# Optimization experiments

Measured on AMD Instinct MI355X. Metric: run time of the kernel, lower is better.

## Reference

```python
import jax, jax.numpy as jnp
import numpy as np

B = 65536
NODE, ENUM, ETYPE = 4, 6, 5
XDIM, EDIM, HDIM, ZDIM = 4, 5, 128, 32
ODIM = (2 * NODE + ETYPE) * ENUM  # 78
BETA = 0.005
EPS_SCALE = 0.01


def setup_inputs() -> dict:
    keys = jax.random.split(jax.random.key(0), 64)
    ki = iter(range(64))
    def rn(shape, s=1.0):
        return jax.random.normal(keys[next(ki)], shape, dtype=jnp.float32) * s
    # NAS-Bench-201 DAG edges per graph, batched as disjoint union
    base_src = jnp.array([0, 0, 1, 0, 1, 2], dtype=jnp.int32)
    base_dst = jnp.array([1, 2, 2, 3, 3, 3], dtype=jnp.int32)
    off = (jnp.arange(B, dtype=jnp.int32) * NODE)[:, None]
    edge_index = jnp.stack([(off + base_src).reshape(-1), (off + base_dst).reshape(-1)])
    s = 0.05
    inp = {
        'x': rn((B * NODE, XDIM)),
        'edge_attr': rn((B * ENUM, EDIM)),
        'arch_tensor': jax.random.uniform(keys[next(ki)], (B, ENUM, 2 * NODE + ETYPE), dtype=jnp.float32),
        'eps': rn((B, ZDIM)),
        'edge_index': edge_index,
        # conv0 (xdim=4 -> hdim=128)
        'c0_rw1': rn((XDIM, XDIM), s), 'c0_rb1': jnp.zeros((XDIM,), jnp.float32),
        'c0_rw2': rn((XDIM, HDIM), s), 'c0_rb2': jnp.zeros((HDIM,), jnp.float32),
        'c0_kw': rn((2 * XDIM + EDIM, HDIM), s),
        # conv1, conv2 (128 -> 128)
        'c1_rw1': rn((HDIM, HDIM), s), 'c1_rb1': jnp.zeros((HDIM,), jnp.float32),
        'c1_rw2': rn((HDIM, HDIM), s), 'c1_rb2': jnp.zeros((HDIM,), jnp.float32),
        'c1_kw': rn((2 * HDIM + EDIM, HDIM), s),
        'c2_rw1': rn((HDIM, HDIM), s), 'c2_rb1': jnp.zeros((HDIM,), jnp.float32),
        'c2_rw2': rn((HDIM, HDIM), s), 'c2_rb2': jnp.zeros((HDIM,), jnp.float32),
        'c2_kw': rn((2 * HDIM + EDIM, HDIM), s),
        # VAE heads
        'fc3_w': rn((HDIM, ZDIM), s), 'fc3_b': jnp.zeros((ZDIM,), jnp.float32),
        'fc4_w': rn((HDIM, ZDIM), s), 'fc4_b': jnp.zeros((ZDIM,), jnp.float32),
        'fc5_w': rn((ZDIM, HDIM), s), 'fc5_b': jnp.zeros((HDIM,), jnp.float32),
        # decoder: Resid_MLP(hdim,hdim) -> Resid_MLP(hdim,odim)
        'd1_mw': rn((HDIM, HDIM), s), 'd1_mb': jnp.zeros((HDIM,), jnp.float32),
        'd1_rw': rn((HDIM, HDIM), s), 'd1_rb': jnp.zeros((HDIM,), jnp.float32),
        'd2_mw': rn((HDIM, ODIM), s), 'd2_mb': jnp.zeros((ODIM,), jnp.float32),
        'd2_rw': rn((HDIM, ODIM), s), 'd2_rb': jnp.zeros((ODIM,), jnp.float32),
    }
    return inp


def _ce(logits, labels):
    # mean cross-entropy over batch*edges, like F.cross_entropy(..., reduction='mean')
    ls = jax.nn.log_softmax(logits, axis=-1)
    return -jnp.mean(jnp.take_along_axis(ls, labels[..., None], axis=-1))


def reference(x, edge_attr, arch_tensor, eps, edge_index,
              c0_rw1, c0_rb1, c0_rw2, c0_rb2, c0_kw,
              c1_rw1, c1_rb1, c1_rw2, c1_rb2, c1_kw,
              c2_rw1, c2_rb1, c2_rw2, c2_rb2, c2_kw,
              fc3_w, fc3_b, fc4_w, fc4_b, fc5_w, fc5_b,
              d1_mw, d1_mb, d1_rw, d1_rb, d2_mw, d2_mb, d2_rw, d2_rb):
    src, dst = edge_index[0], edge_index[1]
    n_nodes = x.shape[0]

    def conv(h, rw1, rb1, rw2, rb2, kw):
        resid = (h @ rw1 + rb1) @ rw2 + rb2  # residual_mlp: two Linears, no activation
        # message: leaky_relu(Linear(cat[x_i(target), x_j(source), edge_attr]))
        m = jax.nn.leaky_relu(jnp.concatenate([h[dst], h[src], edge_attr], axis=1) @ kw)
        return resid + jax.ops.segment_sum(m, dst, num_segments=n_nodes)  # aggr='add'

    h = conv(x, c0_rw1, c0_rb1, c0_rw2, c0_rb2, c0_kw)
    h = conv(h, c1_rw1, c1_rb1, c1_rw2, c1_rb2, c1_kw)
    h = conv(h, c2_rw1, c2_rb1, c2_rw2, c2_rb2, c2_kw)

    hg = h.reshape(B, NODE, HDIM).sum(axis=1)  # sum-pool nodes per graph
    mu = hg @ fc3_w + fc3_b
    logvar = hg @ fc4_w + fc4_b

    # reparameterize (training): z = (eps*eps_scale)*std + mu
    z = eps * EPS_SCALE * jnp.exp(0.5 * logvar) + mu

    # decode
    Hg = jnp.tanh(z @ fc5_w + fc5_b)
    h1 = jax.nn.leaky_relu(Hg @ d1_mw + d1_mb) + (Hg @ d1_rw + d1_rb)
    pred = jax.nn.leaky_relu(h1 @ d2_mw + d2_mb) + (h1 @ d2_rw + d2_rb)
    pred = pred.reshape(B, ENUM, 2 * NODE + ETYPE)
    in_pred, out_pred, et_pred = pred[:, :, :NODE], pred[:, :, NODE:2 * NODE], pred[:, :, 2 * NODE:]

    ti = jnp.argmax(arch_tensor[:, :, :NODE], axis=2)
    to = jnp.argmax(arch_tensor[:, :, NODE:2 * NODE], axis=2)
    te = jnp.argmax(arch_tensor[:, :, 2 * NODE:], axis=2)

    res = _ce(et_pred, te) + _ce(in_pred, ti) + _ce(out_pred, to)
    kld = -0.5 * jnp.mean(1.0 + logvar - mu ** 2 - jnp.exp(logvar))
    return res + BETA * kld
```

## Files before the change

### kernel.cpp

```cpp
#include <hip/hip_runtime.h>
#include <hip/hip_bf16.h>

#define BATCH 65536

typedef __bf16 bf16_t;
typedef __bf16 bf16x8 __attribute__((ext_vector_type(8)));
typedef float  f32x4  __attribute__((ext_vector_type(4)));

__device__ __forceinline__ f32x4 mfma16(bf16x8 a, bf16x8 b, f32x4 c) {
    return __builtin_amdgcn_mfma_f32_16x16x32_bf16(a, b, c, 0, 0, 0);
}
__device__ __forceinline__ int swz128(int row, int col) {
    return row * 128 + ((((col >> 3) ^ (row & 7)) << 3) | (col & 7));
}

struct PrepSrcs { const float* p[16]; };

__global__ __launch_bounds__(256) void prep_weights(PrepSrcs ps,
    const float* __restrict__ c0_rb1, const float* __restrict__ c0_rb2,
    const float* __restrict__ c1_rb1, const float* __restrict__ c1_rb2,
    const float* __restrict__ c2_rb1, const float* __restrict__ c2_rb2,
    bf16_t* __restrict__ dst, float* __restrict__ bias)
{
    int f = blockIdx.x;
    if (f >= 368) {
        int c = threadIdx.x;
        if (c < 128) {
            if (f == 368) {
                const float* rw2 = ps.p[11];
                float s = c1_rb2[c];
                for (int m = 0; m < 128; m++) s += c1_rb1[m] * rw2[m * 128 + c];
                bias[c] = s;
            } else if (f == 369) {
                const float* rw2 = ps.p[13];
                float s = c2_rb2[c];
                for (int m = 0; m < 128; m++) s += c2_rb1[m] * rw2[m * 128 + c];
                bias[128 + c] = s;
            } else {
                const float* rw2 = ps.p[15];
                float s = c0_rb2[c];
                for (int m = 0; m < 4; m++) s += c0_rb1[m] * rw2[m * 128 + c];
                bias[256 + c] = s;
            }
        }
        return;
    }
    const int BASE[20] = {0,32,64,96,128,160,192,200,208,216,248,280,300,320,328,336,344,352,360,368};
    const int SRC[19]  = {10,0,0,12,1,1,2,3,4,5,6,7,8,14,9,9,9,0,1};
    const int KTt[19]  = {4,4,4,4,4,4,4,4,1,4,4,4,4,1,1,1,1,1,1};
    const int KLIM[19] = {128,128,128,128,128,128,128,128,32,128,128,128,128,4,4,4,5,5,5};
    const int NLIM[19] = {128,128,128,128,128,128,32,32,128,128,128,78,78,128,128,128,128,128,128};
    const int STR[19]  = {128,128,128,128,128,128,32,32,128,128,128,78,78,128,128,128,128,128,128};
    const int RO[19]   = {0,0,128,0,0,128,0,0,0,0,0,0,0,0,0,4,8,256,256};

    int ei = 0;
    while (ei < 18 && BASE[ei + 1] <= f) ei++;
    int lf = f - BASE[ei];
    int kt = lf % KTt[ei];
    int nt = lf / KTt[ei];
    #pragma unroll
    for (int r2 = 0; r2 < 2; r2++) {
        int idx = threadIdx.x * 2 + r2;
        int l = idx >> 3, j = idx & 7;
        int row = 32 * kt + 8 * (l >> 4) + j;
        int col = 16 * nt + (l & 15);
        float v = 0.f;
        if (ei == 0 || ei == 3) {
            const float* rw1 = ps.p[ei == 0 ? 10 : 12];
            const float* rw2 = ps.p[ei == 0 ? 11 : 13];
            for (int m = 0; m < 128; m++) v += rw1[row * 128 + m] * rw2[m * 128 + col];
        } else if (ei == 13) {
            if (row < 4) {
                const float* rw1 = ps.p[14];
                const float* rw2 = ps.p[15];
                for (int m = 0; m < 4; m++) v += rw1[row * 4 + m] * rw2[m * 128 + col];
            }
        } else {
            if (row < KLIM[ei] && col < NLIM[ei])
                v = ps.p[SRC[ei]][(row + RO[ei]) * STR[ei] + col];
        }
        dst[f * 512 + idx] = (bf16_t)v;
    }
}

__device__ __forceinline__ void edge_update(float o[4], const f32x4& kd, const f32x4& ks,
                                            const float* et)
{
    float mm;
    mm = kd[1] + ks[0] + et[0]; mm = fmaxf(mm, 0.01f * mm); o[1] += mm;
    mm = kd[2] + ks[0] + et[1]; mm = fmaxf(mm, 0.01f * mm); o[2] += mm;
    mm = kd[2] + ks[1] + et[2]; mm = fmaxf(mm, 0.01f * mm); o[2] += mm;
    mm = kd[3] + ks[0] + et[3]; mm = fmaxf(mm, 0.01f * mm); o[3] += mm;
    mm = kd[3] + ks[1] + et[4]; mm = fmaxf(mm, 0.01f * mm); o[3] += mm;
    mm = kd[3] + ks[2] + et[5]; mm = fmaxf(mm, 0.01f * mm); o[3] += mm;
}

__device__ __forceinline__ void compute_et(bf16_t* etb, const bf16x8* aet,
                                           const bf16_t* wet, int nt,
                                           int w, int q, int lr, int lane)
{
    bf16x8 be = *(const bf16x8*)(wet + nt * 512 + lane * 8);
    #pragma unroll
    for (int t = 0; t < 3; t++) {
        f32x4 z = {0.f, 0.f, 0.f, 0.f};
        z = mfma16(aet[t], be, z);
        #pragma unroll
        for (int j = 0; j < 4; j++)
            etb[(48 * w + 16 * t + 4 * q + j) * 20 + lr] = (bf16_t)z[j];
    }
}

template<bool LAST>
__device__ __forceinline__ void conv_pass(
    bf16_t* lA, bf16_t* etb, const bf16x8* aet,
    const bf16_t* wf, const bf16_t* wet, const float* b12,
    int w, int q, int lr, int lane)
{
    bf16x8 ah[2][4];
    #pragma unroll
    for (int mt = 0; mt < 2; mt++) {
        int row = 32 * w + 16 * mt + lr;
        #pragma unroll
        for (int kt = 0; kt < 4; kt++)
            ah[mt][kt] = *(const bf16x8*)(lA + row * 128 + (((4 * kt + q) ^ (row & 7)) << 3));
    }
    __syncthreads();

    const bf16_t* wfd = wf + 32 * 512;
    const bf16_t* wfs = wf + 64 * 512;
    #pragma unroll 1
    for (int nt = 0; nt < 8; nt++) {
        int col = 16 * nt + lr;
        compute_et(etb, aet, wet, nt, w, q, lr, lane);
        float bv = b12[col];
        f32x4 rr[2], kd[2], ks[2];
        rr[0] = (f32x4){bv, bv, bv, bv}; rr[1] = rr[0];
        kd[0] = (f32x4){0.f, 0.f, 0.f, 0.f}; kd[1] = kd[0];
        ks[0] = kd[0]; ks[1] = kd[0];
        #pragma unroll
        for (int kt = 0; kt < 4; kt++) {
            bf16x8 bw = *(const bf16x8*)(wf  + (nt * 4 + kt) * 512 + lane * 8);
            bf16x8 bd = *(const bf16x8*)(wfd + (nt * 4 + kt) * 512 + lane * 8);
            bf16x8 bs = *(const bf16x8*)(wfs + (nt * 4 + kt) * 512 + lane * 8);
            #pragma unroll
            for (int mt = 0; mt < 2; mt++) {
                rr[mt] = mfma16(ah[mt][kt], bw, rr[mt]);
                kd[mt] = mfma16(ah[mt][kt], bd, kd[mt]);
                ks[mt] = mfma16(ah[mt][kt], bs, ks[mt]);
            }
        }
        #pragma unroll
        for (int mt = 0; mt < 2; mt++) {
            int el = 8 * w + 4 * mt + q;
            float et6[6];
            #pragma unroll
            for (int u = 0; u < 6; u++)
                et6[u] = (float)etb[(48 * w + 24 * mt + 6 * q + u) * 20 + lr];
            float o[4] = {rr[mt][0], rr[mt][1], rr[mt][2], rr[mt][3]};
            edge_update(o, kd[mt], ks[mt], et6);
            if (!LAST) {
                #pragma unroll
                for (int j = 0; j < 4; j++)
                    lA[swz128(32 * w + 16 * mt + 4 * q + j, col)] = (bf16_t)o[j];
            } else {
                lA[swz128(el, col)] = (bf16_t)(o[0] + o[1] + o[2] + o[3]);
            }
        }
    }
    __syncthreads();
}

__device__ __forceinline__ float ce_group(const float* p, const float* a, int off, int len) {
    float m = p[off];
    #pragma unroll
    for (int i = 1; i < 5; i++) if (i < len) m = fmaxf(m, p[off + i]);
    float am = a[off]; int lbl = 0;
    #pragma unroll
    for (int i = 1; i < 5; i++) if (i < len) { float av = a[off + i]; if (av > am) { am = av; lbl = i; } }
    float s = 0.f;
    #pragma unroll
    for (int i = 0; i < 5; i++) if (i < len) s += __expf(p[off + i] - m);
    return (m + __logf(s)) - p[off + lbl];
}

__global__ __launch_bounds__(256, 3) void fused_kernel(
    const float* __restrict__ x, const float* __restrict__ ea,
    const float* __restrict__ arch, const float* __restrict__ eps,
    const bf16_t* __restrict__ wfr, const float* __restrict__ bias,
    const float* __restrict__ fc3_b, const float* __restrict__ fc4_b,
    const float* __restrict__ fc5_b, const float* __restrict__ d1_mb,
    const float* __restrict__ d1_rb, const float* __restrict__ d2_mb,
    const float* __restrict__ d2_rb,
    float* __restrict__ ce_part, float* __restrict__ kld_part)
{
    __shared__ __align__(16) bf16_t lA[128 * 128];
    __shared__ __align__(16) bf16_t etb[192 * 20];

    const int tid = threadIdx.x;
    const int w = tid >> 6, lane = tid & 63, q = lane >> 4, lr = lane & 15;
    const int e0 = blockIdx.x * 32;
    const int r0 = e0 * 4;

    bf16x8 aet[3];
    #pragma unroll
    for (int t = 0; t < 3; t++) {
        bf16x8 a = {0, 0, 0, 0, 0, 0, 0, 0};
        if (q == 0) {
            int e = 48 * w + 16 * t + lr;
            const float* pe = ea + ((size_t)e0 * 6 + e) * 5;
            #pragma unroll
            for (int i = 0; i < 5; i++) a[i] = (bf16_t)pe[i];
        }
        aet[t] = a;
    }

    {
        bf16x8 ax[2];
        #pragma unroll
        for (int mt = 0; mt < 2; mt++) {
            float4 xv = {0.f, 0.f, 0.f, 0.f};
            if (q == 0) xv = *(const float4*)(x + (size_t)(r0 + 32 * w + 16 * mt + lr) * 4);
            bf16x8 a = {0, 0, 0, 0, 0, 0, 0, 0};
            a[0] = (bf16_t)xv.x; a[1] = (bf16_t)xv.y; a[2] = (bf16_t)xv.z; a[3] = (bf16_t)xv.w;
            ax[mt] = a;
        }
        const bf16_t* w0f = wfr + 320 * 512;
        const bf16_t* wdf = wfr + 328 * 512;
        const bf16_t* wsf = wfr + 336 * 512;
        const bf16_t* wef = wfr + 344 * 512;
        const float* b0 = bias + 256;
        #pragma unroll 1
        for (int nt = 0; nt < 8; nt++) {
            int col = 16 * nt + lr;
            compute_et(etb, aet, wef, nt, w, q, lr, lane);
            float bb = b0[col];
            f32x4 rr[2], kd[2], ks[2];
            rr[0] = (f32x4){bb, bb, bb, bb}; rr[1] = rr[0];
            kd[0] = (f32x4){0.f, 0.f, 0.f, 0.f}; kd[1] = kd[0];
            ks[0] = kd[0]; ks[1] = kd[0];
            bf16x8 bw0 = *(const bf16x8*)(w0f + nt * 512 + lane * 8);
            bf16x8 bwa = *(const bf16x8*)(wdf + nt * 512 + lane * 8);
            bf16x8 bwb = *(const bf16x8*)(wsf + nt * 512 + lane * 8);
            #pragma unroll
            for (int mt = 0; mt < 2; mt++) {
                rr[mt] = mfma16(ax[mt], bw0, rr[mt]);
                kd[mt] = mfma16(ax[mt], bwa, kd[mt]);
                ks[mt] = mfma16(ax[mt], bwb, ks[mt]);
            }
            #pragma unroll
            for (int mt = 0; mt < 2; mt++) {
                float et6[6];
                #pragma unroll
                for (int u = 0; u < 6; u++)
                    et6[u] = (float)etb[(48 * w + 24 * mt + 6 * q + u) * 20 + lr];
                float o[4] = {rr[mt][0], rr[mt][1], rr[mt][2], rr[mt][3]};
                edge_update(o, kd[mt], ks[mt], et6);
                #pragma unroll
                for (int j = 0; j < 4; j++)
                    lA[swz128(32 * w + 16 * mt + 4 * q + j, col)] = (bf16_t)o[j];
            }
        }
    }
    __syncthreads();

    conv_pass<false>(lA, etb, aet, wfr,            wfr + 352 * 512, bias,       w, q, lr, lane);
    conv_pass<true >(lA, etb, aet, wfr + 96 * 512, wfr + 360 * 512, bias + 128, w, q, lr, lane);

    const int mtd = w >> 1, tp = w & 1;
    const int grow = 16 * mtd + lr;

    bf16x8 ag[4];
    #pragma unroll
    for (int kt = 0; kt < 4; kt++)
        ag[kt] = *(const bf16x8*)(lA + grow * 128 + (((4 * kt + q) ^ (grow & 7)) << 3));
    float bmu = fc3_b[16 * tp + lr], blv = fc4_b[16 * tp + lr];
    f32x4 amu = (f32x4){bmu, bmu, bmu, bmu}, alv = (f32x4){blv, blv, blv, blv};
    const bf16_t* f3 = wfr + (192 + tp * 4) * 512;
    const bf16_t* f4 = wfr + (200 + tp * 4) * 512;
    #pragma unroll
    for (int kt = 0; kt < 4; kt++) {
        amu = mfma16(ag[kt], *(const bf16x8*)(f3 + kt * 512 + lane * 8), amu);
        alv = mfma16(ag[kt], *(const bf16x8*)(f4 + kt * 512 + lane * 8), alv);
    }
    float kldp = 0.f;
    bf16_t* lz = lA + 4096;
    #pragma unroll
    for (int j = 0; j < 4; j++) {
        int el = 16 * mtd + 4 * q + j;
        float mu = amu[j], lv = alv[j];
        kldp += 1.f + lv - mu * mu - __expf(lv);
        int c = 16 * tp + lr;
        float zz = eps[(size_t)(e0 + el) * 32 + c] * 0.01f * __expf(0.5f * lv) + mu;
        lz[el * 32 + ((((c >> 3) ^ (el & 3)) << 3) | (c & 7))] = (bf16_t)zz;
    }
    __syncthreads();

    bf16_t* lHg = lA + 6144;
    bf16x8 az = *(const bf16x8*)(lz + grow * 32 + ((q ^ (grow & 3)) << 3));
    const bf16_t* f5 = wfr + 208 * 512;
    #pragma unroll 1
    for (int i = 0; i < 4; i++) {
        int nt = 4 * tp + i;
        float b = fc5_b[16 * nt + lr];
        f32x4 a = (f32x4){b, b, b, b};
        a = mfma16(az, *(const bf16x8*)(f5 + nt * 512 + lane * 8), a);
        #pragma unroll
        for (int j = 0; j < 4; j++) {
            float ex2 = __expf(2.f * a[j]);
            float th = 1.f - 2.f / (ex2 + 1.f);
            lHg[swz128(16 * mtd + 4 * q + j, 16 * nt + lr)] = (bf16_t)th;
        }
    }
    __syncthreads();

    bf16x8 aHg[4];
    #pragma unroll
    for (int kt = 0; kt < 4; kt++)
        aHg[kt] = *(const bf16x8*)(lHg + grow * 128 + (((4 * kt + q) ^ (grow & 7)) << 3));
    const bf16_t* wd1m = wfr + 216 * 512;
    const bf16_t* wd1r = wfr + 248 * 512;
    #pragma unroll 1
    for (int i = 0; i < 4; i++) {
        int nt = 4 * tp + i;
        int col = 16 * nt + lr;
        float bm = d1_mb[col], br = d1_rb[col];
        f32x4 am = (f32x4){bm, bm, bm, bm}, ar = (f32x4){br, br, br, br};
        #pragma unroll
        for (int kt = 0; kt < 4; kt++) {
            am = mfma16(aHg[kt], *(const bf16x8*)(wd1m + (nt * 4 + kt) * 512 + lane * 8), am);
            ar = mfma16(aHg[kt], *(const bf16x8*)(wd1r + (nt * 4 + kt) * 512 + lane * 8), ar);
        }
        #pragma unroll
        for (int j = 0; j < 4; j++) {
            float v = fmaxf(am[j], 0.01f * am[j]) + ar[j];
            lA[swz128(16 * mtd + 4 * q + j, col)] = (bf16_t)v;
        }
    }
    __syncthreads();

    bf16x8 a1[4];
    #pragma unroll
    for (int kt = 0; kt < 4; kt++)
        a1[kt] = *(const bf16x8*)(lA + grow * 128 + (((4 * kt + q) ^ (grow & 7)) << 3));
    float* lpred = (float*)(lA + 10240);
    const bf16_t* wd2m = wfr + 280 * 512;
    const bf16_t* wd2r = wfr + 300 * 512;
    const int ntbeg = tp ? 3 : 0, ntend = tp ? 5 : 3;
    #pragma unroll 1
    for (int nt = ntbeg; nt < ntend; nt++) {
        int col = 16 * nt + lr;
        float bm = (col < 78) ? d2_mb[col] : 0.f;
        float br = (col < 78) ? d2_rb[col] : 0.f;
        f32x4 pm = (f32x4){bm, bm, bm, bm}, pr = (f32x4){br, br, br, br};
        #pragma unroll
        for (int kt = 0; kt < 4; kt++) {
            pm = mfma16(a1[kt], *(const bf16x8*)(wd2m + (nt * 4 + kt) * 512 + lane * 8), pm);
            pr = mfma16(a1[kt], *(const bf16x8*)(wd2r + (nt * 4 + kt) * 512 + lane * 8), pr);
        }
        #pragma unroll
        for (int j = 0; j < 4; j++) {
            float v = fmaxf(pm[j], 0.01f * pm[j]) + pr[j];
            lpred[(16 * mtd + 4 * q + j) * 80 + col] = v;
        }
    }
    __syncthreads();

    float ces = 0.f;
    if (tid < 192) {
        int el = tid / 6, u = tid - el * 6;
        const float* pa = arch + ((size_t)(e0 + el) * 6 + u) * 13;
        const float* pp = lpred + el * 80 + u * 13;
        ces  = ce_group(pp, pa, 0, 4);
        ces += ce_group(pp, pa, 4, 4);
        ces += ce_group(pp, pa, 8, 5);
    }
    __syncthreads();
    float* lred = (float*)etb;
    lred[tid] = ces;
    __syncthreads();
    for (int s = 128; s > 0; s >>= 1) {
        if (tid < s) lred[tid] += lred[tid + s];
        __syncthreads();
    }
    if (tid == 0) ce_part[blockIdx.x] = lred[0];
    __syncthreads();
    lred[tid] = kldp;
    __syncthreads();
    for (int s = 128; s > 0; s >>= 1) {
        if (tid < s) lred[tid] += lred[tid + s];
        __syncthreads();
    }
    if (tid == 0) kld_part[blockIdx.x] = lred[0];
}

__global__ __launch_bounds__(256) void final_reduce(
    const float* __restrict__ ce_part, const float* __restrict__ kld_part,
    float* __restrict__ out)
{
    __shared__ float r[256];
    int tid = threadIdx.x;
    float c = 0.f, k = 0.f;
    for (int i = tid; i < 2048; i += 256) { c += ce_part[i]; k += kld_part[i]; }
    r[tid] = c; __syncthreads();
    for (int s = 128; s > 0; s >>= 1) { if (tid < s) r[tid] += r[tid + s]; __syncthreads(); }
    float ctot = r[0];
    __syncthreads();
    r[tid] = k; __syncthreads();
    for (int s = 128; s > 0; s >>= 1) { if (tid < s) r[tid] += r[tid + s]; __syncthreads(); }
    if (tid == 0) {
        float ktot = r[0];
        out[0] = ctot / (65536.f * 6.f) - 0.5f * 0.005f * (ktot / (65536.f * 32.f));
    }
}

extern "C" void kernel_launch(void* const* d_in, const int* in_sizes, int n_in,
                              void* d_out, int out_size, void* d_ws, size_t ws_size,
                              hipStream_t stream)
{
    const float* x      = (const float*)d_in[0];
    const float* ea     = (const float*)d_in[1];
    const float* arch   = (const float*)d_in[2];
    const float* eps    = (const float*)d_in[3];
    const float* c0_rw1 = (const float*)d_in[5];
    const float* c0_rb1 = (const float*)d_in[6];
    const float* c0_rw2 = (const float*)d_in[7];
    const float* c0_rb2 = (const float*)d_in[8];
    const float* c0_kw  = (const float*)d_in[9];
    const float* c1_rw1 = (const float*)d_in[10];
    const float* c1_rb1 = (const float*)d_in[11];
    const float* c1_rw2 = (const float*)d_in[12];
    const float* c1_rb2 = (const float*)d_in[13];
    const float* c1_kw  = (const float*)d_in[14];
    const float* c2_rw1 = (const float*)d_in[15];
    const float* c2_rb1 = (const float*)d_in[16];
    const float* c2_rw2 = (const float*)d_in[17];
    const float* c2_rb2 = (const float*)d_in[18];
    const float* c2_kw  = (const float*)d_in[19];
    const float* fc3_w  = (const float*)d_in[20];
    const float* fc3_b  = (const float*)d_in[21];
    const float* fc4_w  = (const float*)d_in[22];
    const float* fc4_b  = (const float*)d_in[23];
    const float* fc5_w  = (const float*)d_in[24];
    const float* fc5_b  = (const float*)d_in[25];
    const float* d1_mw  = (const float*)d_in[26];
    const float* d1_mb  = (const float*)d_in[27];
    const float* d1_rw  = (const float*)d_in[28];
    const float* d1_rb  = (const float*)d_in[29];
    const float* d2_mw  = (const float*)d_in[30];
    const float* d2_mb  = (const float*)d_in[31];
    const float* d2_rw  = (const float*)d_in[32];
    const float* d2_rb  = (const float*)d_in[33];

    bf16_t* wfr      = (bf16_t*)d_ws;
    float*  bias     = (float*)((char*)d_ws + 376832);
    float*  ce_part  = (float*)((char*)d_ws + 378368);
    float*  kld_part = (float*)((char*)d_ws + 386560);

    PrepSrcs ps;
    ps.p[0] = c1_kw;  ps.p[1] = c2_kw;  ps.p[2] = fc3_w;  ps.p[3] = fc4_w;
    ps.p[4] = fc5_w;  ps.p[5] = d1_mw;  ps.p[6] = d1_rw;  ps.p[7] = d2_mw;
    ps.p[8] = d2_rw;  ps.p[9] = c0_kw;  ps.p[10] = c1_rw1; ps.p[11] = c1_rw2;
    ps.p[12] = c2_rw1; ps.p[13] = c2_rw2; ps.p[14] = c0_rw1; ps.p[15] = c0_rw2;

    prep_weights<<<371, 256, 0, stream>>>(ps, c0_rb1, c0_rb2, c1_rb1, c1_rb2,
                                          c2_rb1, c2_rb2, wfr, bias);
    fused_kernel<<<BATCH / 32, 256, 0, stream>>>(
        x, ea, arch, eps, wfr, bias,
        fc3_b, fc4_b, fc5_b, d1_mb, d1_rb, d2_mb, d2_rb,
        ce_part, kld_part);
    final_reduce<<<1, 256, 0, stream>>>(ce_part, kld_part, (float*)d_out);
}
```

Before: 129.7 us.

## Keep edge-type MFMA results in registers and use wave-shuffle block reductions

Edge-attribute rows are reordered when loaded so that each lane's edge-type MFMA output lines up directly with the edge rows it later consumes. This removes the etb shared-memory staging buffer and its store/load round trip. The two tree reductions over shared memory, each with many barriers, become wave-level xor shuffles plus a small 8-float shared array. The rest of the kernel uses less LDS, but correctness now depends on the new lane-to-edge mapping matching the accumulator layout.

```diff
diff --git a/kernel.cpp b/kernel.cpp
--- a/kernel.cpp
+++ b/kernel.cpp
@@ -95,24 +95,10 @@
     mm = kd[3] + ks[2] + et[5]; mm = fmaxf(mm, 0.01f * mm); o[3] += mm;
 }
 
-__device__ __forceinline__ void compute_et(bf16_t* etb, const bf16x8* aet,
-                                           const bf16_t* wet, int nt,
-                                           int w, int q, int lr, int lane)
-{
-    bf16x8 be = *(const bf16x8*)(wet + nt * 512 + lane * 8);
-    #pragma unroll
-    for (int t = 0; t < 3; t++) {
-        f32x4 z = {0.f, 0.f, 0.f, 0.f};
-        z = mfma16(aet[t], be, z);
-        #pragma unroll
-        for (int j = 0; j < 4; j++)
-            etb[(48 * w + 16 * t + 4 * q + j) * 20 + lr] = (bf16_t)z[j];
-    }
-}
 
 template<bool LAST>
 __device__ __forceinline__ void conv_pass(
-    bf16_t* lA, bf16_t* etb, const bf16x8* aet,
+    bf16_t* lA, const bf16x8 aet[3],
     const bf16_t* wf, const bf16_t* wet, const float* b12,
     int w, int q, int lr, int lane)
 {
@@ -131,12 +117,16 @@
     #pragma unroll 1
     for (int nt = 0; nt < 8; nt++) {
         int col = 16 * nt + lr;
-        compute_et(etb, aet, wet, nt, w, q, lr, lane);
+        const f32x4 zz = {0.f, 0.f, 0.f, 0.f};
+        bf16x8 be = *(const bf16x8*)(wet + nt * 512 + lane * 8);
+        f32x4 zet0 = mfma16(aet[0], be, zz);
+        f32x4 zet1 = mfma16(aet[1], be, zz);
+        f32x4 zetB = mfma16(aet[2], be, zz);
         float bv = b12[col];
         f32x4 rr[2], kd[2], ks[2];
         rr[0] = (f32x4){bv, bv, bv, bv}; rr[1] = rr[0];
-        kd[0] = (f32x4){0.f, 0.f, 0.f, 0.f}; kd[1] = kd[0];
-        ks[0] = kd[0]; ks[1] = kd[0];
+        kd[0] = zz; kd[1] = zz;
+        ks[0] = zz; ks[1] = zz;
         #pragma unroll
         for (int kt = 0; kt < 4; kt++) {
             bf16x8 bw = *(const bf16x8*)(wf  + (nt * 4 + kt) * 512 + lane * 8);
@@ -152,10 +142,9 @@
         #pragma unroll
         for (int mt = 0; mt < 2; mt++) {
             int el = 8 * w + 4 * mt + q;
-            float et6[6];
-            #pragma unroll
-            for (int u = 0; u < 6; u++)
-                et6[u] = (float)etb[(48 * w + 24 * mt + 6 * q + u) * 20 + lr];
+            f32x4 zA = mt ? zet1 : zet0;
+            float et6[6] = {zA[0], zA[1], zA[2], zA[3],
+                            mt ? zetB[2] : zetB[0], mt ? zetB[3] : zetB[1]};
             float o[4] = {rr[mt][0], rr[mt][1], rr[mt][2], rr[mt][3]};
             edge_update(o, kd[mt], ks[mt], et6);
             if (!LAST) {
@@ -194,7 +183,7 @@
     float* __restrict__ ce_part, float* __restrict__ kld_part)
 {
     __shared__ __align__(16) bf16_t lA[128 * 128];
-    __shared__ __align__(16) bf16_t etb[192 * 20];
+    __shared__ __align__(16) float  lred[8];
 
     const int tid = threadIdx.x;
     const int w = tid >> 6, lane = tid & 63, q = lane >> 4, lr = lane & 15;
@@ -206,8 +195,10 @@
     for (int t = 0; t < 3; t++) {
         bf16x8 a = {0, 0, 0, 0, 0, 0, 0, 0};
         if (q == 0) {
-            int e = 48 * w + 16 * t + lr;
-            const float* pe = ea + ((size_t)e0 * 6 + e) * 5;
+            int el_w, u;
+            if (t < 2) { el_w = 4 * t + (lr >> 2); u = lr & 3; }
+            else       { el_w = 4 * ((lr >> 1) & 1) + (lr >> 2); u = 4 + (lr & 1); }
+            const float* pe = ea + (size_t)((e0 + 8 * w + el_w) * 6 + u) * 5;
             #pragma unroll
             for (int i = 0; i < 5; i++) a[i] = (bf16_t)pe[i];
         }
@@ -232,12 +223,16 @@
         #pragma unroll 1
         for (int nt = 0; nt < 8; nt++) {
             int col = 16 * nt + lr;
-            compute_et(etb, aet, wef, nt, w, q, lr, lane);
+            const f32x4 zz = {0.f, 0.f, 0.f, 0.f};
+            bf16x8 be = *(const bf16x8*)(wef + nt * 512 + lane * 8);
+            f32x4 zet0 = mfma16(aet[0], be, zz);
+            f32x4 zet1 = mfma16(aet[1], be, zz);
+            f32x4 zetB = mfma16(aet[2], be, zz);
             float bb = b0[col];
             f32x4 rr[2], kd[2], ks[2];
             rr[0] = (f32x4){bb, bb, bb, bb}; rr[1] = rr[0];
-            kd[0] = (f32x4){0.f, 0.f, 0.f, 0.f}; kd[1] = kd[0];
-            ks[0] = kd[0]; ks[1] = kd[0];
+            kd[0] = zz; kd[1] = zz;
+            ks[0] = zz; ks[1] = zz;
             bf16x8 bw0 = *(const bf16x8*)(w0f + nt * 512 + lane * 8);
             bf16x8 bwa = *(const bf16x8*)(wdf + nt * 512 + lane * 8);
             bf16x8 bwb = *(const bf16x8*)(wsf + nt * 512 + lane * 8);
@@ -249,10 +244,9 @@
             }
             #pragma unroll
             for (int mt = 0; mt < 2; mt++) {
-                float et6[6];
-                #pragma unroll
-                for (int u = 0; u < 6; u++)
-                    et6[u] = (float)etb[(48 * w + 24 * mt + 6 * q + u) * 20 + lr];
+                f32x4 zA = mt ? zet1 : zet0;
+                float et6[6] = {zA[0], zA[1], zA[2], zA[3],
+                                mt ? zetB[2] : zetB[0], mt ? zetB[3] : zetB[1]};
                 float o[4] = {rr[mt][0], rr[mt][1], rr[mt][2], rr[mt][3]};
                 edge_update(o, kd[mt], ks[mt], et6);
                 #pragma unroll
@@ -263,8 +257,8 @@
     }
     __syncthreads();
 
-    conv_pass<false>(lA, etb, aet, wfr,            wfr + 352 * 512, bias,       w, q, lr, lane);
-    conv_pass<true >(lA, etb, aet, wfr + 96 * 512, wfr + 360 * 512, bias + 128, w, q, lr, lane);
+    conv_pass<false>(lA, aet, wfr,            wfr + 352 * 512, bias,       w, q, lr, lane);
+    conv_pass<true >(lA, aet, wfr + 96 * 512, wfr + 360 * 512, bias + 128, w, q, lr, lane);
 
     const int mtd = w >> 1, tp = w & 1;
     const int grow = 16 * mtd + lr;
@@ -290,8 +284,8 @@
         float mu = amu[j], lv = alv[j];
         kldp += 1.f + lv - mu * mu - __expf(lv);
         int c = 16 * tp + lr;
-        float zz = eps[(size_t)(e0 + el) * 32 + c] * 0.01f * __expf(0.5f * lv) + mu;
-        lz[el * 32 + ((((c >> 3) ^ (el & 3)) << 3) | (c & 7))] = (bf16_t)zz;
+        float zz2 = eps[(size_t)(e0 + el) * 32 + c] * 0.01f * __expf(0.5f * lv) + mu;
+        lz[el * 32 + ((((c >> 3) ^ (el & 3)) << 3) | (c & 7))] = (bf16_t)zz2;
     }
     __syncthreads();
 
@@ -374,23 +368,17 @@
         ces += ce_group(pp, pa, 4, 4);
         ces += ce_group(pp, pa, 8, 5);
     }
-    __syncthreads();
-    float* lred = (float*)etb;
-    lred[tid] = ces;
-    __syncthreads();
-    for (int s = 128; s > 0; s >>= 1) {
-        if (tid < s) lred[tid] += lred[tid + s];
-        __syncthreads();
-    }
-    if (tid == 0) ce_part[blockIdx.x] = lred[0];
-    __syncthreads();
-    lred[tid] = kldp;
-    __syncthreads();
-    for (int s = 128; s > 0; s >>= 1) {
-        if (tid < s) lred[tid] += lred[tid + s];
-        __syncthreads();
-    }
-    if (tid == 0) kld_part[blockIdx.x] = lred[0];
+    #pragma unroll
+    for (int m2 = 1; m2 < 64; m2 <<= 1) {
+        ces  += __shfl_xor(ces, m2, 64);
+        kldp += __shfl_xor(kldp, m2, 64);
+    }
+    if (lane == 0) { lred[w] = ces; lred[4 + w] = kldp; }
+    __syncthreads();
+    if (tid == 0) {
+        ce_part[blockIdx.x]  = lred[0] + lred[1] + lred[2] + lred[3];
+        kld_part[blockIdx.x] = lred[4] + lred[5] + lred[6] + lred[7];
+    }
 }
 
 __global__ __launch_bounds__(256) void final_reduce(
```

Result: no change. 127.3 us (-1.9%).
